# Kernel optimization log

Hardware: AMD Instinct MI355X
Metric: run time of the kernel (lower is better)

## Reference

```python
import jax, jax.numpy as jnp
import numpy as np

IN_F = 135; D = 512; K = 10; DCT_N = 34; IN_N = 120; OUT_N = 24
VL = K + OUT_N          # 34, window length
VN = IN_N - K - OUT_N + 1  # 87, number of windows
NSTAGE = 2
BN_SCALE = 1.0 / np.sqrt(1.0 + 1e-5)  # eval-mode BN with default running stats (mean 0, var 1)


def get_dct_matrix(N):
    dct_m = np.eye(N)
    for k in range(N):
        for i in range(N):
            w = np.sqrt(2.0 / N)
            if k == 0:
                w = np.sqrt(1.0 / N)
            dct_m[k, i] = w * np.cos(np.pi * (i + 0.5) * k / N)
    idct_m = np.linalg.inv(dct_m)
    return dct_m, idct_m

_DCT_NP, _IDCT_NP = get_dct_matrix(VL)
DCT = jnp.asarray(_DCT_NP[:DCT_N], dtype=jnp.float32)        # [34,34] (dct_n == vl)
IDCT = jnp.asarray(_IDCT_NP[:, :DCT_N], dtype=jnp.float32)   # [34,34]

WIN_IDX = np.arange(VL)[None, :] + np.arange(VN)[:, None]    # [87,34]
PAD_IDX = np.concatenate([np.arange(IN_N - K, IN_N), np.full(OUT_N, IN_N - 1)])  # last 10 frames + last frame repeated


def conv1d(x, w):
    return jax.lax.conv_general_dilated(x, w, (1,), 'VALID',
                                        dimension_numbers=('NCH', 'OIH', 'NCH'))


def gconv(x, att, w, b):
    # GraphConvolution: att @ (x @ w) + b ; x: [b,n,f_in]
    return jnp.einsum('nm,bmf->bnf', att, x @ w) + b


def bn_eval(y, g, b):
    bs, n, f = y.shape
    v = y.reshape(bs, n * f)
    v = g * (v * BN_SCALE) + b
    return v.reshape(bs, n, f)


def setup_inputs() -> dict:
    key = jax.random.key(0)
    ks = jax.random.split(key, 20)
    s = 0.05  # small init scale so tanh/att stay in sane range
    return {
        'poses':    jax.random.normal(ks[0], (256, 144, 135), jnp.float32),
        'qw1':      jax.random.normal(ks[1], (512, 135, 6)) * s,
        'qw2':      jax.random.normal(ks[2], (512, 512, 5)) * s,
        'kw1':      jax.random.normal(ks[3], (512, 135, 6)) * s,
        'kw2':      jax.random.normal(ks[4], (512, 512, 5)) * s,
        'gc1_att':  jax.random.normal(ks[5], (135, 135)) * s,
        'gc1_w':    jax.random.normal(ks[6], (68, 512)) * s,
        'gc1_b':    jax.random.normal(ks[7], (512,)) * s,
        'bn1_g':    jnp.ones((69120,), jnp.float32),
        'bn1_b':    jnp.zeros((69120,), jnp.float32),
        'gcb_att':  jax.random.normal(ks[8], (4, 135, 135)) * s,
        'gcb_w':    jax.random.normal(ks[9], (4, 512, 512)) * s,
        'gcb_b':    jax.random.normal(ks[10], (4, 512)) * s,
        'gcb_g':    jnp.ones((4, 69120), jnp.float32),
        'gcb_beta': jnp.zeros((4, 69120), jnp.float32),
        'gc7_att':  jax.random.normal(ks[11], (135, 135)) * s,
        'gc7_w':    jax.random.normal(ks[12], (512, 68)) * s,
        'gc7_b':    jax.random.normal(ks[13], (68,)) * s,
    }


def reference(poses, qw1, qw2, kw1, kw2,
              gc1_att, gc1_w, gc1_b, bn1_g, bn1_b,
              gcb_att, gcb_w, gcb_b, gcb_g, gcb_beta,
              gc7_att, gc7_w, gc7_b):
    src = poses[:, :IN_N]                      # [b,120,135]
    bs = src.shape[0]
    src_t = jnp.transpose(src, (0, 2, 1))      # [b,135,120]
    key_in = src_t[:, :, :IN_N - OUT_N] / 1000.0   # [b,135,96]
    qry_in = src_t[:, :, -K:] / 1000.0             # [b,135,10]

    key_f = jax.nn.relu(conv1d(jax.nn.relu(conv1d(key_in, kw1)), kw2))  # [b,512,87]
    qry_f = jax.nn.relu(conv1d(jax.nn.relu(conv1d(qry_in, qw1)), qw2))  # [b,512,1]

    # non-softmax attention: matmul + eps-normalize
    score = jnp.einsum('bdq,bdk->bqk', qry_f, key_f) + 1e-15   # [b,1,87]
    att = score / jnp.sum(score, axis=2, keepdims=True)

    # overlapping windows -> DCT of each window
    windows = src[:, WIN_IDX]                                   # [b,87,34,135]
    val = jnp.einsum('kt,bvtf->bvfk', DCT, windows).reshape(bs, VN, IN_F * DCT_N)
    dct_att = jnp.einsum('bqv,bvz->bqz', att, val)[:, 0].reshape(bs, IN_F, DCT_N)

    input_gcn = src[:, PAD_IDX]                                 # [b,34,135]
    dct_in = jnp.einsum('kt,btf->bfk', DCT, input_gcn)          # [b,135,34]
    x = jnp.concatenate([dct_in, dct_att], axis=-1)             # [b,135,68]

    # GCN (eval mode: dropout = identity, BN uses running stats)
    y = jnp.tanh(bn_eval(gconv(x, gc1_att, gc1_w, gc1_b), bn1_g, bn1_b))
    for i in range(NSTAGE):
        res = y
        h = jnp.tanh(bn_eval(gconv(y, gcb_att[2 * i], gcb_w[2 * i], gcb_b[2 * i]),
                             gcb_g[2 * i], gcb_beta[2 * i]))
        h = jnp.tanh(bn_eval(gconv(h, gcb_att[2 * i + 1], gcb_w[2 * i + 1], gcb_b[2 * i + 1]),
                             gcb_g[2 * i + 1], gcb_beta[2 * i + 1]))
        y = h + res
    y = gconv(y, gc7_att, gc7_w, gc7_b) + x                     # [b,135,68]

    out = jnp.einsum('tk,bfk->btf', IDCT, y[:, :, :DCT_N])      # [b,34,135]
    preds = out[:, -OUT_N:, :]                                  # [b,24,135]
    return preds
```

## Files before the change

kernel.cpp:

```cpp
#include <hip/hip_runtime.h>
#include <math.h>

#define POSE_ROWS 144
#define NF 135
#define DD 512
#define KQ 10
#define DCTN 34
#define INN 120
#define OUTN 24
#define VN 87
#define BATCH 256
#define RP 34816
#define NODEP 136
#define BN_SCALE 0.9999950000374997f

typedef __attribute__((ext_vector_type(8))) short short8;
typedef __attribute__((ext_vector_type(4))) float floatx4;

static __device__ __forceinline__ ushort f2bf(float f) {
    unsigned u = __builtin_bit_cast(unsigned, f);
    u = (u + 0x7FFFu + ((u >> 16) & 1u)) >> 16;
    return (ushort)u;
}
static __device__ __forceinline__ float bf2f(ushort s) {
    return __builtin_bit_cast(float, (unsigned)s << 16);
}
static __device__ __forceinline__ float tanh_fast(float x) {
    float ax = __builtin_fabsf(x);
    float e = __builtin_amdgcn_exp2f(ax * -2.885390081777927f);
    float t = (1.f - e) * __builtin_amdgcn_rcpf(1.f + e);
    return __builtin_copysignf(t, x);
}

#define GLOAD_LDS(gp, lp) __builtin_amdgcn_global_load_lds( \
    (const __attribute__((address_space(1))) unsigned int*)(const void*)(gp), \
    (__attribute__((address_space(3))) unsigned int*)(void*)(lp), 16, 0, 0)

#define PB_POSES 19584
#define PB_K1B   22912
#define PB_K2B   33152
#define PB_WT1   33408
#define PB_WTB   37504
#define PB_WT7   37640
#define PB_A1    37742
#define PB_AB    38147
#define PB_A7    38249
#define PB_BN    39609
#define PB_Z     39610
#define PB_DCT   39615

__global__ __launch_bounds__(256) void prep_all(
    const float* __restrict__ poses, ushort* __restrict__ pb16,
    const float* __restrict__ kw1, const float* __restrict__ qw1,
    ushort* __restrict__ Wt1k, ushort* __restrict__ Wt1q,
    const float* __restrict__ kw2, const float* __restrict__ qw2,
    ushort* __restrict__ Wt2k, ushort* __restrict__ Wt2q,
    const float* __restrict__ gc1_w, ushort* __restrict__ WT1,
    const float* __restrict__ gcb_w, ushort* __restrict__ WTb,
    const float* __restrict__ gc7_w, ushort* __restrict__ WT7,
    const float* __restrict__ gc1_att, ushort* __restrict__ A16_1,
    const float* __restrict__ gcb_att, ushort* __restrict__ A16_B,
    const float* __restrict__ gc7_att, ushort* __restrict__ A16_7,
    const float* __restrict__ bn1_g, const float* __restrict__ bn1_b,
    const float* __restrict__ gcb_g, const float* __restrict__ gcb_beta,
    float* __restrict__ bnT, float* __restrict__ zpadf, float* __restrict__ dct)
{
    const int blk = blockIdx.x;
    const int tid = threadIdx.x;
    if (blk < PB_POSES) {
        int idx = blk * 256 + tid;
        int i = idx % NODEP;
        int row = (idx / NODEP) % POSE_ROWS;
        int b = idx / (NODEP * POSE_ROWS);
        float v = (i < NF) ? poses[((long long)b * POSE_ROWS + row) * NF + i] * 1e-3f : 0.f;
        pb16[idx] = f2bf(v);
    } else if (blk < PB_K1B) {
        int wi = blk - PB_POSES;
        const float* src = (wi < 1664) ? kw1 : qw1;
        ushort* dst = (wi < 1664) ? Wt1k : Wt1q;
        int idx = (wi % 1664) * 256 + tid;
        int n = idx / 832, k = idx % 832;
        int h = k / 136, i = k % 136;
        float v = (i < 135 && h < 6) ? src[((long long)n * 135 + i) * 6 + h] : 0.f;
        dst[idx] = f2bf(v);
    } else if (blk < PB_K2B) {
        int wi = blk - PB_K1B;
        const float* src = (wi < 5120) ? kw2 : qw2;
        ushort* dst = (wi < 5120) ? Wt2k : Wt2q;
        int idx = (wi % 5120) * 256 + tid;
        int n = idx / 2560, k = idx % 2560;
        int h = k / 512, i = k % 512;
        dst[idx] = f2bf(src[((long long)n * 512 + i) * 5 + h]);
    } else if (blk < PB_WT1) {
        int idx = (blk - PB_K2B) * 256 + tid;
        int n = idx / 128, k = idx % 128;
        WT1[idx] = f2bf((k < 68) ? gc1_w[(long long)k * 512 + n] : 0.f);
    } else if (blk < PB_WTB) {
        int g = (blk - PB_WT1) * 256 + tid;
        int L = g >> 18, idx = g & 262143;
        int n = idx / 512, k = idx % 512;
        WTb[g] = f2bf(gcb_w[(long long)L * 262144 + (long long)k * 512 + n]);
    } else if (blk < PB_WT7) {
        int idx = (blk - PB_WTB) * 256 + tid;
        int n = idx / 512, k = idx % 512;
        WT7[idx] = f2bf(gc7_w[(long long)k * 68 + n]);
    } else if (blk < PB_A1) {
        int idx = (blk - PB_WT7) * 256 + tid;
        if (idx < 135 * 192) {
            int r = idx / 192, c = idx % 192;
            A16_1[idx] = f2bf(c < 135 ? gc1_att[r * 135 + c] : 0.f);
        }
    } else if (blk < PB_AB) {
        int idx = (blk - PB_A1) * 256 + tid;
        int r = idx / 192, c = idx % 192;
        A16_B[idx] = f2bf(c < 135 ? gcb_att[r * 135 + c] : 0.f);
    } else if (blk < PB_A7) {
        int idx = (blk - PB_AB) * 256 + tid;
        if (idx < 135 * 192) {
            int r = idx / 192, c = idx % 192;
            A16_7[idx] = f2bf(c < 135 ? gc7_att[r * 135 + c] : 0.f);
        }
    } else if (blk < PB_BN) {
        int g = (blk - PB_A7) * 256 + tid;
        int p = g / 69632, idx = g % 69632;
        int node = idx % 136, m = idx / 136;
        const float* gs = (p == 0) ? bn1_g : (gcb_g + (p - 1) * 69120);
        const float* bs = (p == 0) ? bn1_b : (gcb_beta + (p - 1) * 69120);
        float* gt = bnT + (long long)p * 139264;
        float* bt = gt + 69632;
        gt[idx] = (node < 135) ? gs[node * 512 + m] : 0.f;
        bt[idx] = (node < 135) ? bs[node * 512 + m] : 0.f;
    } else if (blk < PB_Z) {
        if (tid < 128) zpadf[tid] = 0.f;
    } else {
        int idx = (blk - PB_Z) * 256 + tid;
        if (idx < DCTN * DCTN) {
            int k = idx / DCTN, i = idx % DCTN;
            double w = (k == 0) ? sqrt(1.0 / DCTN) : sqrt(2.0 / DCTN);
            dct[idx] = (float)(w * cos(3.14159265358979323846 * (i + 0.5) * k / (double)DCTN));
        }
    }
}

template<int BM, int BN>
__global__ __launch_bounds__(256) void gemm2(
    const ushort* __restrict__ A, const ushort* __restrict__ Bt,
    const ushort* __restrict__ zpad,
    int M, int N, int K,
    int mode, int CNT, int Pc,
    int rpbA, long long sAw, long long sAr, long long sAbz,
    long long sBr, long long sBbz,
    float* __restrict__ C, ushort* __restrict__ C16,
    long long sCbz, long long sCm, long long sCn,
    int do_relu, const float* __restrict__ bias, int bias_mode,
    const float* __restrict__ bnTg, const float* __restrict__ bnTb,
    int do_tanh, const ushort* __restrict__ resid16, const float* __restrict__ resid32)
{
    constexpr int SM = BM / 32, SN = BN / 32;
    constexpr int RA = BM / 32, RB = BN / 32;
    __shared__ ushort As[BM * 64];
    __shared__ ushort Bs[BN * 64];

    int mb, nb;
    if (mode == 0) { mb = blockIdx.y; nb = blockIdx.x; }
    else {
        int gx = blockIdx.x;
        int x = gx & 7, s = gx >> 3;
        if (mode == 1) { mb = s % CNT; nb = x * Pc + s / CNT; }
        else           { nb = s % CNT; mb = x * Pc + s / CNT; }
    }
    const int m0 = mb * BM, n0 = nb * BN;
    if (m0 >= M || n0 >= N) return;

    const int tid = threadIdx.x;
    const int lane = tid & 63, w = tid >> 6;
    const int bz = blockIdx.z;
    const int wm = (w >> 1) * (BM / 2), wn = (w & 1) * (BN / 2);
    const int chunk = (lane & 7) ^ ((lane >> 3) & 7);

    const ushort* pA[RA]; int stA[RA];
    #pragma unroll
    for (int j = 0; j < RA; j++) {
        int m = m0 + j * 32 + w * 8 + (lane >> 3);
        bool v = m < M;
        long long off = v ? ((long long)(m / rpbA) * sAw + (long long)(m % rpbA) * sAr
                            + (long long)bz * sAbz) : 0;
        pA[j] = v ? (A + off + chunk * 8) : (zpad + chunk * 8);
        stA[j] = v ? 64 : 0;
    }
    const ushort* pB[RB]; int stB[RB];
    #pragma unroll
    for (int j = 0; j < RB; j++) {
        int n = n0 + j * 32 + w * 8 + (lane >> 3);
        bool v = n < N;
        long long off = v ? ((long long)n * sBr + (long long)bz * sBbz) : 0;
        pB[j] = v ? (Bt + off + chunk * 8) : (zpad + chunk * 8);
        stB[j] = v ? 64 : 0;
    }

    floatx4 acc[SM][SN];
    #pragma unroll
    for (int i = 0; i < SM; i++)
        #pragma unroll
        for (int j = 0; j < SN; j++)
            acc[i][j] = (floatx4){0.f, 0.f, 0.f, 0.f};

    for (int k0 = 0; k0 < K; k0 += 64) {
        #pragma unroll
        for (int j = 0; j < RA; j++)
            GLOAD_LDS(pA[j], &As[(j * 32 + w * 8) * 64]);
        #pragma unroll
        for (int j = 0; j < RB; j++)
            GLOAD_LDS(pB[j], &Bs[(j * 32 + w * 8) * 64]);
        __syncthreads();

        #pragma unroll
        for (int kk = 0; kk < 2; kk++) {
            short8 af[SM], bf[SN];
            #pragma unroll
            for (int sm = 0; sm < SM; sm++) {
                int lr = wm + sm * 16 + (lane & 15);
                int slot = ((lane >> 4) + kk * 4) ^ (lr & 7);
                af[sm] = *(const short8*)&As[lr * 64 + slot * 8];
            }
            #pragma unroll
            for (int sn = 0; sn < SN; sn++) {
                int lr = wn + sn * 16 + (lane & 15);
                int slot = ((lane >> 4) + kk * 4) ^ (lr & 7);
                bf[sn] = *(const short8*)&Bs[lr * 64 + slot * 8];
            }
            #pragma unroll
            for (int sm = 0; sm < SM; sm++)
                #pragma unroll
                for (int sn = 0; sn < SN; sn++)
                    acc[sm][sn] = __builtin_amdgcn_mfma_f32_16x16x32_bf16(af[sm], bf[sn], acc[sm][sn], 0, 0, 0);
        }
        __syncthreads();

        #pragma unroll
        for (int j = 0; j < RA; j++) pA[j] += stA[j];
        #pragma unroll
        for (int j = 0; j < RB; j++) pB[j] += stB[j];
    }

    const int lc = lane & 15;
    const int lr4 = (lane >> 4) << 2;
    #pragma unroll
    for (int sm = 0; sm < SM; sm++) {
        #pragma unroll
        for (int sn = 0; sn < SN; sn++) {
            int n = n0 + wn + sn * 16 + lc;
            if (n >= N) continue;
            int node = n % 136;
            int mbv = m0 + wm + sm * 16 + lr4;
            float vv[4];
            #pragma unroll
            for (int r = 0; r < 4; r++) {
                int m = mbv + r;
                float v = acc[sm][sn][r];
                if (do_relu) v = fmaxf(v, 0.f);
                if (bias) v += (bias_mode == 1) ? bias[m < M ? m : 0] : bias[n];
                if (bnTg) {
                    long long gi = (long long)(m < M ? m : 0) * 136 + node;
                    v = bnTg[gi] * (v * BN_SCALE) + bnTb[gi];
                }
                if (do_tanh) v = tanh_fast(v);
                long long addr = (long long)bz * sCbz + (long long)m * sCm + (long long)n * sCn;
                if (m < M) {
                    if (resid16) v += bf2f(resid16[addr]);
                    else if (resid32) v += resid32[addr];
                    if (C) C[addr] = v;
                    if (C16 && sCm != 1) C16[addr] = f2bf(v);
                }
                vv[r] = v;
            }
            if (C16 && sCm == 1 && mbv + 3 < M) {
                ushort4 pk;
                pk.x = f2bf(vv[0]); pk.y = f2bf(vv[1]); pk.z = f2bf(vv[2]); pk.w = f2bf(vv[3]);
                *(ushort4*)&C16[(long long)bz * sCbz + mbv + (long long)n * sCn] = pk;
            }
        }
    }
}

__global__ __launch_bounds__(256) void att_k(const float* __restrict__ kf, const float* __restrict__ qf,
                                             float* __restrict__ att) {
    int b = blockIdx.x;
    int tid = threadIdx.x;
    int lane = tid & 63, w = tid >> 6;
    __shared__ float s[96];
    __shared__ float ssum;
    const float* qb = qf + b * DD + lane * 8;
    float4 q0 = *(const float4*)qb;
    float4 q1 = *(const float4*)(qb + 4);
    const float* kb = kf + (long long)b * VN * DD;
    for (int v = w; v < VN; v += 4) {
        const float* kr = kb + v * DD + lane * 8;
        float4 k0 = *(const float4*)kr;
        float4 k1 = *(const float4*)(kr + 4);
        float p = q0.x * k0.x + q0.y * k0.y + q0.z * k0.z + q0.w * k0.w
                + q1.x * k1.x + q1.y * k1.y + q1.z * k1.z + q1.w * k1.w;
        #pragma unroll
        for (int off = 32; off; off >>= 1) p += __shfl_xor(p, off);
        if (lane == 0) s[v] = p + 1e-15f;
    }
    __syncthreads();
    if (tid < 64) {
        float p2 = (tid < VN ? s[tid] : 0.f) + ((tid + 64) < VN ? s[tid + 64] : 0.f);
        #pragma unroll
        for (int off = 32; off; off >>= 1) p2 += __shfl_xor(p2, off);
        if (tid == 0) ssum = p2;
    }
    __syncthreads();
    float inv = 1.f / ssum;
    for (int v = tid; v < VN; v += 256) att[b * VN + v] = s[v] * inv;
}

__global__ void weighted_k(const float* __restrict__ poses, const float* __restrict__ att,
                           float* __restrict__ w34) {
    int t = blockIdx.x;
    int b = blockIdx.y;
    int f = threadIdx.x;
    if (f >= NF) return;
    const float* pb = poses + (long long)b * POSE_ROWS * NF + t * NF + f;
    const float* ab = att + b * VN;
    float acc = 0.f;
    for (int v = 0; v < VN; v++) acc += ab[v] * pb[v * NF];
    w34[(long long)b * DCTN * NF + t * NF + f] = acc;
}

__global__ void build_x(const float* __restrict__ poses, const float* __restrict__ w34,
                        const float* __restrict__ dctm, float* __restrict__ x32,
                        ushort* __restrict__ xT16) {
    int idx = blockIdx.x * 256 + threadIdx.x;
    if (idx >= BATCH * NF * 68) return;
    int kk = idx % 68;
    int f = (idx / 68) % NF;
    int b = idx / (68 * NF);
    float acc = 0.f;
    if (kk < DCTN) {
        const float* pb = poses + (long long)b * POSE_ROWS * NF;
        #pragma unroll
        for (int t = 0; t < DCTN; t++) {
            int row = (t < KQ) ? (INN - KQ + t) : (INN - 1);
            acc += dctm[kk * DCTN + t] * pb[row * NF + f];
        }
    } else {
        int k2 = kk - DCTN;
        const float* wb = w34 + (long long)b * DCTN * NF + f;
        #pragma unroll
        for (int t = 0; t < DCTN; t++) acc += dctm[k2 * DCTN + t] * wb[t * NF];
    }
    long long R = (long long)b * NODEP + f;
    x32[R * 68 + kk] = acc;
    xT16[(long long)kk * RP + R] = f2bf(acc);
}

__global__ void idct_out(const float* __restrict__ h32, const float* __restrict__ dctm,
                         float* __restrict__ out) {
    int idx = blockIdx.x * 256 + threadIdx.x;
    if (idx >= BATCH * OUTN * NF) return;
    int f = idx % NF;
    int t = (idx / NF) % OUTN;
    int b = idx / (NF * OUTN);
    const float* yr = h32 + ((long long)b * NODEP + f) * 68;
    float acc = 0.f;
    #pragma unroll
    for (int k = 0; k < DCTN; k++) acc += dctm[k * DCTN + (KQ + t)] * yr[k];
    out[idx] = acc;
}

extern "C" void kernel_launch(void* const* d_in, const int* in_sizes, int n_in,
                              void* d_out, int out_size, void* d_ws, size_t ws_size,
                              hipStream_t stream) {
    const float* poses   = (const float*)d_in[0];
    const float* qw1     = (const float*)d_in[1];
    const float* qw2     = (const float*)d_in[2];
    const float* kw1     = (const float*)d_in[3];
    const float* kw2     = (const float*)d_in[4];
    const float* gc1_att = (const float*)d_in[5];
    const float* gc1_w   = (const float*)d_in[6];
    const float* gc1_b   = (const float*)d_in[7];
    const float* bn1_g   = (const float*)d_in[8];
    const float* bn1_b   = (const float*)d_in[9];
    const float* gcb_att = (const float*)d_in[10];
    const float* gcb_w   = (const float*)d_in[11];
    const float* gcb_b   = (const float*)d_in[12];
    const float* gcb_g   = (const float*)d_in[13];
    const float* gcb_beta= (const float*)d_in[14];
    const float* gc7_att = (const float*)d_in[15];
    const float* gc7_w   = (const float*)d_in[16];
    const float* gc7_b   = (const float*)d_in[17];
    float* out = (float*)d_out;
    float* w = (float*)d_ws;

    float* dct   = w;
    float* att   = w + 1280;
    float* w34   = w + 23808;
    float* x32   = w + 1198848;
    float* h32   = w + 3566336;
    float* qf    = w + 5933824;
    ushort* su   = (ushort*)(w + 6064896);
    ushort* WT1    = su;
    ushort* WTb    = su + 65536;
    ushort* WT7    = su + 1114112;
    ushort* A16_1  = su + 1148928;
    ushort* A16_B  = su + 1174848;
    ushort* A16_7  = su + 1278528;
    float* bnT   = w + 6717120;
    float* kf    = w + 7413440;
    ushort* R2   = (ushort*)(w + 18816704);
    ushort* yT16  = R2;
    ushort* r1k16 = R2;
    ushort* r1q16 = R2 + 11927552;
    ushort* R3   = (ushort*)(w + 27729600);
    ushort* hT16  = R3;
    ushort* pb16  = R3;
    ushort* Wt1k  = R3 + 5013504;
    ushort* Wt1q  = R3 + 5439488;
    ushort* Wt2k  = R3 + 5865472;
    ushort* Wt2q  = R3 + 7176192;
    ushort* R4   = (ushort*)(w + 36642496);
    ushort* zN16  = R4;
    ushort* xT16  = R4;
    ushort* z116  = R4 + 2367488;
    float* zpadf = w + 45555392;
    const ushort* zpad = (const ushort*)zpadf;

    const int INF_RPB = 1 << 30;

    prep_all<<<PB_DCT, 256, 0, stream>>>(
        poses, pb16, kw1, qw1, Wt1k, Wt1q, kw2, qw2, Wt2k, Wt2q,
        gc1_w, WT1, gcb_w, WTb, gc7_w, WT7,
        gc1_att, A16_1, gcb_att, A16_B, gc7_att, A16_7,
        bn1_g, bn1_b, gcb_g, gcb_beta, bnT, zpadf, dct);

    gemm2<128,64><<<dim3(1472, 1, 1), 256, 0, stream>>>(pb16, Wt1k, zpad, 23296, 512, 832,
        2, 8, 23, 91, 19584LL, 136LL, 0LL, 832LL, 0LL,
        (float*)nullptr, r1k16, 0LL, 512LL, 1LL, 1, nullptr, 0, nullptr, nullptr, 0, nullptr, nullptr);
    gemm2<128,128><<<dim3(4, 10, 1), 256, 0, stream>>>(pb16 + 110*136, Wt1q, zpad, 1280, 512, 832,
        0, 0, 0, 5, 19584LL, 136LL, 0LL, 832LL, 0LL,
        (float*)nullptr, r1q16, 0LL, 512LL, 1LL, 1, nullptr, 0, nullptr, nullptr, 0, nullptr, nullptr);
    gemm2<128,64><<<dim3(1408, 1, 1), 256, 0, stream>>>(r1k16, Wt2k, zpad, 22272, 512, 2560,
        2, 8, 22, 87, 46592LL, 512LL, 0LL, 2560LL, 0LL,
        kf, (ushort*)nullptr, 0LL, 512LL, 1LL, 1, nullptr, 0, nullptr, nullptr, 0, nullptr, nullptr);
    gemm2<64,64><<<dim3(8, 4, 1), 256, 0, stream>>>(r1q16, Wt2q, zpad, 256, 512, 2560,
        0, 0, 0, INF_RPB, 0LL, 2560LL, 0LL, 2560LL, 0LL,
        qf, (ushort*)nullptr, 0LL, 512LL, 1LL, 1, nullptr, 0, nullptr, nullptr, 0, nullptr, nullptr);

    att_k<<<BATCH, 256, 0, stream>>>(kf, qf, att);
    weighted_k<<<dim3(DCTN, BATCH), 192, 0, stream>>>(poses, att, w34);
    build_x<<<(BATCH * NF * 68 + 255) / 256, 256, 0, stream>>>(poses, w34, dct, x32, xT16);

    gemm2<64,64><<<dim3(3, 2, BATCH), 256, 0, stream>>>(xT16, A16_1, zpad, 68, 135, 192,
        0, 0, 0, INF_RPB, 0LL, (long long)RP, 136LL, 192LL, 0LL,
        (float*)nullptr, z116, 10880LL, 1LL, 80LL, 0, nullptr, 0, nullptr, nullptr, 0, nullptr, nullptr);
    gemm2<128,64><<<dim3(2176, 1, 1), 256, 0, stream>>>(WT1, z116, zpad, 512, RP, 128,
        1, 4, 68, INF_RPB, 0LL, 128LL, 0LL, 80LL, 0LL,
        (float*)nullptr, yT16, 0LL, (long long)RP, 1LL, 0, gc1_b, 1, bnT, bnT + 69632, 1, nullptr, nullptr);

    for (int L = 0; L < 4; L++) {
        const ushort* min = (L & 1) ? hT16 : yT16;
        gemm2<64,64><<<dim3(3, 8, BATCH), 256, 0, stream>>>(min, A16_B + L*25920, zpad, 512, 135, 192,
            0, 0, 0, INF_RPB, 0LL, (long long)RP, 136LL, 192LL, 0LL,
            (float*)nullptr, zN16, 69632LL, 1LL, 512LL, 0, nullptr, 0, nullptr, nullptr, 0, nullptr, nullptr);
        gemm2<128,64><<<dim3(2176, 1, 1), 256, 0, stream>>>(WTb + L*262144, zN16, zpad, 512, RP, 512,
            1, 4, 68, INF_RPB, 0LL, 512LL, 0LL, 512LL, 0LL,
            (float*)nullptr, (L & 1) ? yT16 : hT16, 0LL, (long long)RP, 1LL,
            0, gcb_b + L*512, 1, bnT + (1 + L) * 139264, bnT + (1 + L) * 139264 + 69632, 1,
            (L & 1) ? yT16 : (const ushort*)nullptr, nullptr);
    }

    gemm2<64,64><<<dim3(3, 8, BATCH), 256, 0, stream>>>(yT16, A16_7, zpad, 512, 135, 192,
        0, 0, 0, INF_RPB, 0LL, (long long)RP, 136LL, 192LL, 0LL,
        (float*)nullptr, zN16, 69632LL, 1LL, 512LL, 0, nullptr, 0, nullptr, nullptr, 0, nullptr, nullptr);
    gemm2<64,64><<<dim3(1088, 1, 1), 256, 0, stream>>>(zN16, WT7, zpad, RP, 68, 512,
        2, 2, 68, INF_RPB, 0LL, 512LL, 0LL, 512LL, 0LL,
        h32, (ushort*)nullptr, 0LL, 68LL, 1LL, 0, gc7_b, 2, nullptr, nullptr, 0, nullptr, x32);

    idct_out<<<(BATCH * OUTN * NF + 255) / 256, 256, 0, stream>>>(h32, dct, out);
}
```

Baseline: 1.028 ms.

## Double-buffer GEMM LDS tiles, transpose GCN weight GEMMs, store keys as bf16

The GEMM main loop now double-buffers its LDS tiles, so the global-to-LDS load for the next K step is issued before the current step is computed, hiding memory latency at the cost of twice the shared memory. The GCN weight GEMMs swap operands so activations become the M side, and the BN gamma/beta tables are kept in natural node-major layout through a new bn_mode index path. The key-feature GEMM writes bf16 instead of fp32, and att_k reads bf16, halving that traffic but lowering precision. The query conv GEMM also moves to a smaller 64x64 tile.

```diff
diff --git a/kernel.cpp b/kernel.cpp
--- a/kernel.cpp
+++ b/kernel.cpp
@@ -63,7 +63,7 @@
     const float* __restrict__ gc7_att, ushort* __restrict__ A16_7,
     const float* __restrict__ bn1_g, const float* __restrict__ bn1_b,
     const float* __restrict__ gcb_g, const float* __restrict__ gcb_beta,
-    float* __restrict__ bnT, float* __restrict__ zpadf, float* __restrict__ dct)
+    float* __restrict__ bnN, float* __restrict__ zpadf, float* __restrict__ dct)
 {
     const int blk = blockIdx.x;
     const int tid = threadIdx.x;
@@ -123,13 +123,13 @@
     } else if (blk < PB_BN) {
         int g = (blk - PB_A7) * 256 + tid;
         int p = g / 69632, idx = g % 69632;
-        int node = idx % 136, m = idx / 136;
+        int node = idx / 512;
         const float* gs = (p == 0) ? bn1_g : (gcb_g + (p - 1) * 69120);
         const float* bs = (p == 0) ? bn1_b : (gcb_beta + (p - 1) * 69120);
-        float* gt = bnT + (long long)p * 139264;
+        float* gt = bnN + (long long)p * 139264;
         float* bt = gt + 69632;
-        gt[idx] = (node < 135) ? gs[node * 512 + m] : 0.f;
-        bt[idx] = (node < 135) ? bs[node * 512 + m] : 0.f;
+        gt[idx] = (node < 135) ? gs[idx] : 0.f;
+        bt[idx] = (node < 135) ? bs[idx] : 0.f;
     } else if (blk < PB_Z) {
         if (tid < 128) zpadf[tid] = 0.f;
     } else {
@@ -153,13 +153,15 @@
     float* __restrict__ C, ushort* __restrict__ C16,
     long long sCbz, long long sCm, long long sCn,
     int do_relu, const float* __restrict__ bias, int bias_mode,
-    const float* __restrict__ bnTg, const float* __restrict__ bnTb,
+    const float* __restrict__ bnTg, const float* __restrict__ bnTb, int bn_mode,
     int do_tanh, const ushort* __restrict__ resid16, const float* __restrict__ resid32)
 {
     constexpr int SM = BM / 32, SN = BN / 32;
     constexpr int RA = BM / 32, RB = BN / 32;
-    __shared__ ushort As[BM * 64];
-    __shared__ ushort Bs[BN * 64];
+    __shared__ ushort As0[BM * 64];
+    __shared__ ushort Bs0[BN * 64];
+    __shared__ ushort As1[BM * 64];
+    __shared__ ushort Bs1[BN * 64];
 
     int mb, nb;
     if (mode == 0) { mb = blockIdx.y; nb = blockIdx.x; }
@@ -205,43 +207,57 @@
         for (int j = 0; j < SN; j++)
             acc[i][j] = (floatx4){0.f, 0.f, 0.f, 0.f};
 
-    for (int k0 = 0; k0 < K; k0 += 64) {
-        #pragma unroll
-        for (int j = 0; j < RA; j++)
-            GLOAD_LDS(pA[j], &As[(j * 32 + w * 8) * 64]);
-        #pragma unroll
-        for (int j = 0; j < RB; j++)
-            GLOAD_LDS(pB[j], &Bs[(j * 32 + w * 8) * 64]);
+    #define ISSUE(ASB, BSB) do {                                          \
+        _Pragma("unroll")                                                 \
+        for (int j = 0; j < RA; j++) {                                    \
+            GLOAD_LDS(pA[j], &ASB[(j * 32 + w * 8) * 64]);                \
+            pA[j] += stA[j];                                              \
+        }                                                                 \
+        _Pragma("unroll")                                                 \
+        for (int j = 0; j < RB; j++) {                                    \
+            GLOAD_LDS(pB[j], &BSB[(j * 32 + w * 8) * 64]);                \
+            pB[j] += stB[j];                                              \
+        }                                                                 \
+    } while (0)
+    #define COMPUTE(ASB, BSB) do {                                        \
+        _Pragma("unroll")                                                 \
+        for (int kk = 0; kk < 2; kk++) {                                  \
+            short8 af[SM], bf[SN];                                        \
+            _Pragma("unroll")                                             \
+            for (int sm = 0; sm < SM; sm++) {                             \
+                int lr = wm + sm * 16 + (lane & 15);                      \
+                int slot = ((lane >> 4) + kk * 4) ^ (lr & 7);             \
+                af[sm] = *(const short8*)&ASB[lr * 64 + slot * 8];        \
+            }                                                             \
+            _Pragma("unroll")                                             \
+            for (int sn = 0; sn < SN; sn++) {                             \
+                int lr = wn + sn * 16 + (lane & 15);                      \
+                int slot = ((lane >> 4) + kk * 4) ^ (lr & 7);             \
+                bf[sn] = *(const short8*)&BSB[lr * 64 + slot * 8];        \
+            }                                                             \
+            _Pragma("unroll")                                             \
+            for (int sm = 0; sm < SM; sm++)                               \
+                _Pragma("unroll")                                         \
+                for (int sn = 0; sn < SN; sn++)                           \
+                    acc[sm][sn] = __builtin_amdgcn_mfma_f32_16x16x32_bf16(af[sm], bf[sn], acc[sm][sn], 0, 0, 0); \
+        }                                                                 \
+    } while (0)
+
+    const int nit = K >> 6;
+    ISSUE(As0, Bs0);
+    for (int it = 0; it < nit; ) {
         __syncthreads();
-
-        #pragma unroll
-        for (int kk = 0; kk < 2; kk++) {
-            short8 af[SM], bf[SN];
-            #pragma unroll
-            for (int sm = 0; sm < SM; sm++) {
-                int lr = wm + sm * 16 + (lane & 15);
-                int slot = ((lane >> 4) + kk * 4) ^ (lr & 7);
-                af[sm] = *(const short8*)&As[lr * 64 + slot * 8];
-            }
-            #pragma unroll
-            for (int sn = 0; sn < SN; sn++) {
-                int lr = wn + sn * 16 + (lane & 15);
-                int slot = ((lane >> 4) + kk * 4) ^ (lr & 7);
-                bf[sn] = *(const short8*)&Bs[lr * 64 + slot * 8];
-            }
-            #pragma unroll
-            for (int sm = 0; sm < SM; sm++)
-                #pragma unroll
-                for (int sn = 0; sn < SN; sn++)
-                    acc[sm][sn] = __builtin_amdgcn_mfma_f32_16x16x32_bf16(af[sm], bf[sn], acc[sm][sn], 0, 0, 0);
-        }
+        if (it + 1 < nit) ISSUE(As1, Bs1);
+        COMPUTE(As0, Bs0);
+        it++;
+        if (it == nit) break;
         __syncthreads();
-
-        #pragma unroll
-        for (int j = 0; j < RA; j++) pA[j] += stA[j];
-        #pragma unroll
-        for (int j = 0; j < RB; j++) pB[j] += stB[j];
-    }
+        if (it + 1 < nit) ISSUE(As0, Bs0);
+        COMPUTE(As1, Bs1);
+        it++;
+    }
+    #undef ISSUE
+    #undef COMPUTE
 
     const int lc = lane & 15;
     const int lr4 = (lane >> 4) << 2;
@@ -251,7 +267,6 @@
         for (int sn = 0; sn < SN; sn++) {
             int n = n0 + wn + sn * 16 + lc;
             if (n >= N) continue;
-            int node = n % 136;
             int mbv = m0 + wm + sm * 16 + lr4;
             float vv[4];
             #pragma unroll
@@ -261,7 +276,10 @@
                 if (do_relu) v = fmaxf(v, 0.f);
                 if (bias) v += (bias_mode == 1) ? bias[m < M ? m : 0] : bias[n];
                 if (bnTg) {
-                    long long gi = (long long)(m < M ? m : 0) * 136 + node;
+                    int ms = m < M ? m : 0;
+                    long long gi = (bn_mode == 1)
+                        ? (long long)ms * 136 + (n % 136)
+                        : (long long)(ms % 136) * 512 + n;
                     v = bnTg[gi] * (v * BN_SCALE) + bnTb[gi];
                 }
                 if (do_tanh) v = tanh_fast(v);
@@ -283,7 +301,7 @@
     }
 }
 
-__global__ __launch_bounds__(256) void att_k(const float* __restrict__ kf, const float* __restrict__ qf,
+__global__ __launch_bounds__(256) void att_k(const ushort* __restrict__ kf, const float* __restrict__ qf,
                                              float* __restrict__ att) {
     int b = blockIdx.x;
     int tid = threadIdx.x;
@@ -291,15 +309,15 @@
     __shared__ float s[96];
     __shared__ float ssum;
     const float* qb = qf + b * DD + lane * 8;
-    float4 q0 = *(const float4*)qb;
-    float4 q1 = *(const float4*)(qb + 4);
-    const float* kb = kf + (long long)b * VN * DD;
+    float qv[8];
+    *(float4*)&qv[0] = *(const float4*)qb;
+    *(float4*)&qv[4] = *(const float4*)(qb + 4);
+    const ushort* kb = kf + (long long)b * VN * DD;
     for (int v = w; v < VN; v += 4) {
-        const float* kr = kb + v * DD + lane * 8;
-        float4 k0 = *(const float4*)kr;
-        float4 k1 = *(const float4*)(kr + 4);
-        float p = q0.x * k0.x + q0.y * k0.y + q0.z * k0.z + q0.w * k0.w
-                + q1.x * k1.x + q1.y * k1.y + q1.z * k1.z + q1.w * k1.w;
+        short8 k8 = *(const short8*)(kb + v * DD + lane * 8);
+        float p = 0.f;
+        #pragma unroll
+        for (int j = 0; j < 8; j++) p += qv[j] * bf2f((ushort)k8[j]);
         #pragma unroll
         for (int off = 32; off; off >>= 1) p += __shfl_xor(p, off);
         if (lane == 0) s[v] = p + 1e-15f;
@@ -407,8 +425,8 @@
     ushort* A16_1  = su + 1148928;
     ushort* A16_B  = su + 1174848;
     ushort* A16_7  = su + 1278528;
-    float* bnT   = w + 6717120;
-    float* kf    = w + 7413440;
+    float* bnN   = w + 6717120;
+    ushort* kf16 = (ushort*)(w + 7413440);
     ushort* R2   = (ushort*)(w + 18816704);
     ushort* yT16  = R2;
     ushort* r1k16 = R2;
@@ -433,50 +451,50 @@
         poses, pb16, kw1, qw1, Wt1k, Wt1q, kw2, qw2, Wt2k, Wt2q,
         gc1_w, WT1, gcb_w, WTb, gc7_w, WT7,
         gc1_att, A16_1, gcb_att, A16_B, gc7_att, A16_7,
-        bn1_g, bn1_b, gcb_g, gcb_beta, bnT, zpadf, dct);
+        bn1_g, bn1_b, gcb_g, gcb_beta, bnN, zpadf, dct);
 
     gemm2<128,64><<<dim3(1472, 1, 1), 256, 0, stream>>>(pb16, Wt1k, zpad, 23296, 512, 832,
         2, 8, 23, 91, 19584LL, 136LL, 0LL, 832LL, 0LL,
-        (float*)nullptr, r1k16, 0LL, 512LL, 1LL, 1, nullptr, 0, nullptr, nullptr, 0, nullptr, nullptr);
-    gemm2<128,128><<<dim3(4, 10, 1), 256, 0, stream>>>(pb16 + 110*136, Wt1q, zpad, 1280, 512, 832,
+        (float*)nullptr, r1k16, 0LL, 512LL, 1LL, 1, nullptr, 0, nullptr, nullptr, 0, 0, nullptr, nullptr);
+    gemm2<64,64><<<dim3(8, 20, 1), 256, 0, stream>>>(pb16 + 110*136, Wt1q, zpad, 1280, 512, 832,
         0, 0, 0, 5, 19584LL, 136LL, 0LL, 832LL, 0LL,
-        (float*)nullptr, r1q16, 0LL, 512LL, 1LL, 1, nullptr, 0, nullptr, nullptr, 0, nullptr, nullptr);
+        (float*)nullptr, r1q16, 0LL, 512LL, 1LL, 1, nullptr, 0, nullptr, nullptr, 0, 0, nullptr, nullptr);
     gemm2<128,64><<<dim3(1408, 1, 1), 256, 0, stream>>>(r1k16, Wt2k, zpad, 22272, 512, 2560,
         2, 8, 22, 87, 46592LL, 512LL, 0LL, 2560LL, 0LL,
-        kf, (ushort*)nullptr, 0LL, 512LL, 1LL, 1, nullptr, 0, nullptr, nullptr, 0, nullptr, nullptr);
+        (float*)nullptr, kf16, 0LL, 512LL, 1LL, 1, nullptr, 0, nullptr, nullptr, 0, 0, nullptr, nullptr);
     gemm2<64,64><<<dim3(8, 4, 1), 256, 0, stream>>>(r1q16, Wt2q, zpad, 256, 512, 2560,
         0, 0, 0, INF_RPB, 0LL, 2560LL, 0LL, 2560LL, 0LL,
-        qf, (ushort*)nullptr, 0LL, 512LL, 1LL, 1, nullptr, 0, nullptr, nullptr, 0, nullptr, nullptr);
-
-    att_k<<<BATCH, 256, 0, stream>>>(kf, qf, att);
+        qf, (ushort*)nullptr, 0LL, 512LL, 1LL, 1, nullptr, 0, nullptr, nullptr, 0, 0, nullptr, nullptr);
+
+    att_k<<<BATCH, 256, 0, stream>>>(kf16, qf, att);
     weighted_k<<<dim3(DCTN, BATCH), 192, 0, stream>>>(poses, att, w34);
     build_x<<<(BATCH * NF * 68 + 255) / 256, 256, 0, stream>>>(poses, w34, dct, x32, xT16);
 
     gemm2<64,64><<<dim3(3, 2, BATCH), 256, 0, stream>>>(xT16, A16_1, zpad, 68, 135, 192,
         0, 0, 0, INF_RPB, 0LL, (long long)RP, 136LL, 192LL, 0LL,
-        (float*)nullptr, z116, 10880LL, 1LL, 80LL, 0, nullptr, 0, nullptr, nullptr, 0, nullptr, nullptr);
-    gemm2<128,64><<<dim3(2176, 1, 1), 256, 0, stream>>>(WT1, z116, zpad, 512, RP, 128,
-        1, 4, 68, INF_RPB, 0LL, 128LL, 0LL, 80LL, 0LL,
-        (float*)nullptr, yT16, 0LL, (long long)RP, 1LL, 0, gc1_b, 1, bnT, bnT + 69632, 1, nullptr, nullptr);
+        (float*)nullptr, z116, 10880LL, 1LL, 80LL, 0, nullptr, 0, nullptr, nullptr, 0, 0, nullptr, nullptr);
+    gemm2<128,64><<<dim3(2176, 1, 1), 256, 0, stream>>>(z116, WT1, zpad, RP, 512, 128,
+        2, 8, 34, 136, 10880LL, 80LL, 0LL, 128LL, 0LL,
+        (float*)nullptr, yT16, 0LL, 1LL, (long long)RP, 0, gc1_b, 2, bnN, bnN + 69632, 2, 1, nullptr, nullptr);
 
     for (int L = 0; L < 4; L++) {
         const ushort* min = (L & 1) ? hT16 : yT16;
         gemm2<64,64><<<dim3(3, 8, BATCH), 256, 0, stream>>>(min, A16_B + L*25920, zpad, 512, 135, 192,
             0, 0, 0, INF_RPB, 0LL, (long long)RP, 136LL, 192LL, 0LL,
-            (float*)nullptr, zN16, 69632LL, 1LL, 512LL, 0, nullptr, 0, nullptr, nullptr, 0, nullptr, nullptr);
-        gemm2<128,64><<<dim3(2176, 1, 1), 256, 0, stream>>>(WTb + L*262144, zN16, zpad, 512, RP, 512,
-            1, 4, 68, INF_RPB, 0LL, 512LL, 0LL, 512LL, 0LL,
-            (float*)nullptr, (L & 1) ? yT16 : hT16, 0LL, (long long)RP, 1LL,
-            0, gcb_b + L*512, 1, bnT + (1 + L) * 139264, bnT + (1 + L) * 139264 + 69632, 1,
+            (float*)nullptr, zN16, 69632LL, 1LL, 512LL, 0, nullptr, 0, nullptr, nullptr, 0, 0, nullptr, nullptr);
+        gemm2<128,64><<<dim3(2176, 1, 1), 256, 0, stream>>>(zN16, WTb + L*262144, zpad, RP, 512, 512,
+            2, 8, 34, 136, 69632LL, 512LL, 0LL, 512LL, 0LL,
+            (float*)nullptr, (L & 1) ? yT16 : hT16, 0LL, 1LL, (long long)RP,
+            0, gcb_b + L*512, 2, bnN + (1 + L) * 139264, bnN + (1 + L) * 139264 + 69632, 2, 1,
             (L & 1) ? yT16 : (const ushort*)nullptr, nullptr);
     }
 
     gemm2<64,64><<<dim3(3, 8, BATCH), 256, 0, stream>>>(yT16, A16_7, zpad, 512, 135, 192,
         0, 0, 0, INF_RPB, 0LL, (long long)RP, 136LL, 192LL, 0LL,
-        (float*)nullptr, zN16, 69632LL, 1LL, 512LL, 0, nullptr, 0, nullptr, nullptr, 0, nullptr, nullptr);
+        (float*)nullptr, zN16, 69632LL, 1LL, 512LL, 0, nullptr, 0, nullptr, nullptr, 0, 0, nullptr, nullptr);
     gemm2<64,64><<<dim3(1088, 1, 1), 256, 0, stream>>>(zN16, WT7, zpad, RP, 68, 512,
-        2, 2, 68, INF_RPB, 0LL, 512LL, 0LL, 512LL, 0LL,
-        h32, (ushort*)nullptr, 0LL, 68LL, 1LL, 0, gc7_b, 2, nullptr, nullptr, 0, nullptr, x32);
+        2, 2, 68, 136, 69632LL, 512LL, 0LL, 512LL, 0LL,
+        h32, (ushort*)nullptr, 0LL, 68LL, 1LL, 0, gc7_b, 2, nullptr, nullptr, 0, 0, nullptr, x32);
 
     idct_out<<<(BATCH * OUTN * NF + 255) / 256, 256, 0, stream>>>(h32, dct, out);
 }
```

Measured after the change: 1.207 ms. 17.4% more time.
